# Kernel tuning notes

Hardware: AMD Instinct MI355X
Metric: run time of the kernel (lower is better)

## Reference

```python
import jax, jax.numpy as jnp
import numpy as np

C = 64          # channels
N = 500000      # points
FILTERS = (1, 3, 3, 3, 1)
INIT_SCALE = 8.0
LIKELIHOOD_BOUND = 1e-9


def setup_inputs() -> dict:
    key = jax.random.key(0)
    ks = jax.random.split(key, 6)
    inputs = jax.random.normal(ks[0], (N, C), jnp.float32) * 4.0
    # deterministic replacement for torch's np.random.uniform(-0.5, 0.5) noise
    noise = jax.random.uniform(ks[1], (N, C), jnp.float32, minval=-0.5, maxval=0.5)
    d = {"inputs": inputs, "noise": noise}
    scale = INIT_SCALE ** (1.0 / (len(FILTERS) - 1))  # init_scale**(1/4)
    for i in range(4):
        fo, fi = FILTERS[i + 1], FILTERS[i]
        init_m = float(np.log(np.expm1(1.0 / scale / fo)))
        d[f"m{i}"] = jnp.full((C, fo, fi), init_m, dtype=jnp.float32)
        d[f"b{i}"] = jax.random.uniform(ks[2 + i], (C, fo, 1), jnp.float32, minval=-0.5, maxval=0.5)
        d[f"f{i}"] = jnp.zeros((C, fo, 1), jnp.float32)
    return d


@jax.custom_vjp
def low_bound(x):
    return jnp.clip(x, LIKELIHOOD_BOUND)

def _lb_fwd(x):
    return jnp.clip(x, LIKELIHOOD_BOUND), x

def _lb_bwd(x, g):
    # torch Low_bound: grad zeroed where x < 1e-9 (the g<0 pass-through is
    # nullified by the preceding hard zeroing in the original code)
    return (jnp.where(x >= LIKELIHOOD_BOUND, g, jnp.zeros_like(g)),)

low_bound.defvjp(_lb_fwd, _lb_bwd)


def _logits_cumulative(x, ms, bs, fs):
    # x: (C, 1, N); each layer: tiny per-channel matmul + bias + tanh gate
    logits = x
    for m, b, f in zip(ms, bs, fs):
        logits = jnp.einsum('cij,cjn->cin', jax.nn.softplus(m), logits) + b
        logits = logits + jnp.tanh(f) * jnp.tanh(logits)
    return logits


def reference(inputs, noise, m0, m1, m2, m3, b0, b1, b2, b3, f0, f1, f2, f3):
    # quantize_mode='noise': additive uniform noise
    outputs = inputs + noise                       # (N, C)
    x = outputs.T[:, None, :]                      # (C, 1, N)
    ms = (m0, m1, m2, m3)
    bs = (b0, b1, b2, b3)
    fs = (f0, f1, f2, f3)
    lower = _logits_cumulative(x - 0.5, ms, bs, fs)   # (C, 1, N)
    upper = _logits_cumulative(x + 0.5, ms, bs, fs)   # (C, 1, N)
    sign = -jax.lax.stop_gradient(jnp.sign(lower + upper))
    likelihood = jnp.abs(jax.nn.sigmoid(sign * upper) - jax.nn.sigmoid(sign * lower))
    likelihood = likelihood.reshape(C, N).T        # (N, C)
    likelihood = low_bound(likelihood)
    return outputs, likelihood
```

## Files before the change

### kernel.cpp

```cpp
#include <hip/hip_runtime.h>

#define CH 64

__device__ __forceinline__ float frcp(float x) { return __builtin_amdgcn_rcpf(x); }

__device__ __forceinline__ float ftanh(float x) {
    float e = __expf(2.0f * x);
    return 1.0f - 2.0f * frcp(e + 1.0f);
}

__device__ __forceinline__ float softplus_f(float x) {
    float ax = fabsf(x);
    return fmaxf(x, 0.0f) + log1pf(__expf(-ax));
}

__device__ __forceinline__ float chain_gen(float x,
    const float* w0, const float* B0, const float* T0,
    const float* w1, const float* B1, const float* T1,
    const float* w2, const float* B2, const float* T2,
    const float* w3, float B3, float T3)
{
    float l[3], t[3];
#pragma unroll
    for (int i = 0; i < 3; i++) {
        float z = fmaf(w0[i], x, B0[i]);
        l[i] = fmaf(T0[i], ftanh(z), z);
    }
#pragma unroll
    for (int i = 0; i < 3; i++) {
        float z = B1[i];
#pragma unroll
        for (int j = 0; j < 3; j++) z = fmaf(w1[i * 3 + j], l[j], z);
        t[i] = fmaf(T1[i], ftanh(z), z);
    }
#pragma unroll
    for (int i = 0; i < 3; i++) {
        float z = B2[i];
#pragma unroll
        for (int j = 0; j < 3; j++) z = fmaf(w2[i * 3 + j], t[j], z);
        l[i] = fmaf(T2[i], ftanh(z), z);
    }
    float z = B3;
#pragma unroll
    for (int j = 0; j < 3; j++) z = fmaf(w3[j], l[j], z);
    return fmaf(T3, ftanh(z), z);
}

__device__ __forceinline__ float2 chain2_nogate(float xl, float xu,
    const float* w0, const float* B0,
    const float* w1, const float* B1,
    const float* w2, const float* B2,
    const float* w3, float B3)
{
    float lx[3], ly[3], tx[3], ty[3];
#pragma unroll
    for (int i = 0; i < 3; i++) {
        lx[i] = fmaf(w0[i], xl, B0[i]);
        ly[i] = fmaf(w0[i], xu, B0[i]);
    }
#pragma unroll
    for (int i = 0; i < 3; i++) {
        float zx = B1[i], zy = B1[i];
#pragma unroll
        for (int j = 0; j < 3; j++) {
            zx = fmaf(w1[i * 3 + j], lx[j], zx);
            zy = fmaf(w1[i * 3 + j], ly[j], zy);
        }
        tx[i] = zx; ty[i] = zy;
    }
#pragma unroll
    for (int i = 0; i < 3; i++) {
        float zx = B2[i], zy = B2[i];
#pragma unroll
        for (int j = 0; j < 3; j++) {
            zx = fmaf(w2[i * 3 + j], tx[j], zx);
            zy = fmaf(w2[i * 3 + j], ty[j], zy);
        }
        lx[i] = zx; ly[i] = zy;
    }
    float zx = B3, zy = B3;
#pragma unroll
    for (int j = 0; j < 3; j++) {
        zx = fmaf(w3[j], lx[j], zx);
        zy = fmaf(w3[j], ly[j], zy);
    }
    return make_float2(zx, zy);
}

__device__ __forceinline__ float likelihood_f(float lo, float up) {
    lo = fminf(fmaxf(lo, -40.0f), 40.0f);
    up = fminf(fmaxf(up, -40.0f), 40.0f);
    float a = __expf(-up);
    float b = __expf(-lo);
    float num = b - a;
    float den = fmaf(a, b, a) + b + 1.0f;
    float like = fabsf(num * frcp(den));
    return fmaxf(like, 1e-9f);
}

__global__ __launch_bounds__(256) void eb_kernel(
    const float* __restrict__ in, const float* __restrict__ noise,
    const float* __restrict__ m0, const float* __restrict__ b0, const float* __restrict__ f0,
    const float* __restrict__ m1, const float* __restrict__ b1, const float* __restrict__ f1,
    const float* __restrict__ m2, const float* __restrict__ b2, const float* __restrict__ f2,
    const float* __restrict__ m3, const float* __restrict__ b3, const float* __restrict__ f3,
    float* __restrict__ out, int total)
{
    const int tid = blockIdx.x * blockDim.x + threadIdx.x;
    const int c = tid & (CH - 1);

    float w0[3], B0[3], T0[3];
    float w1[9], B1[3], T1[3];
    float w2[9], B2[3], T2[3];
    float w3[3], B3, T3;
#pragma unroll
    for (int i = 0; i < 3; i++) {
        w0[i] = softplus_f(m0[c * 3 + i]);
        B0[i] = b0[c * 3 + i];
        T0[i] = tanhf(f0[c * 3 + i]);
        B1[i] = b1[c * 3 + i];
        T1[i] = tanhf(f1[c * 3 + i]);
        B2[i] = b2[c * 3 + i];
        T2[i] = tanhf(f2[c * 3 + i]);
        w3[i] = softplus_f(m3[c * 3 + i]);
    }
#pragma unroll
    for (int i = 0; i < 9; i++) {
        w1[i] = softplus_f(m1[c * 9 + i]);
        w2[i] = softplus_f(m2[c * 9 + i]);
    }
    B3 = b3[c];
    T3 = tanhf(f3[c]);

    bool gated = (T3 != 0.0f);
#pragma unroll
    for (int i = 0; i < 3; i++)
        gated = gated || (T0[i] != 0.0f) || (T1[i] != 0.0f) || (T2[i] != 0.0f);

    const int stride = gridDim.x * blockDim.x;

    if (!gated) {
        for (int idx = tid; idx < total; idx += stride) {
            float v = in[idx] + noise[idx];
            out[idx] = v;
            float2 r = chain2_nogate(v - 0.5f, v + 0.5f,
                                     w0, B0, w1, B1, w2, B2, w3, B3);
            out[total + idx] = likelihood_f(r.x, r.y);
        }
    } else {
        for (int idx = tid; idx < total; idx += stride) {
            float v = in[idx] + noise[idx];
            out[idx] = v;
            float lo = chain_gen(v - 0.5f, w0, B0, T0, w1, B1, T1, w2, B2, T2, w3, B3, T3);
            float up = chain_gen(v + 0.5f, w0, B0, T0, w1, B1, T1, w2, B2, T2, w3, B3, T3);
            out[total + idx] = likelihood_f(lo, up);
        }
    }
}

extern "C" void kernel_launch(void* const* d_in, const int* in_sizes, int n_in,
                              void* d_out, int out_size, void* d_ws, size_t ws_size,
                              hipStream_t stream) {
    const float* in    = (const float*)d_in[0];
    const float* noise = (const float*)d_in[1];
    const float* m0 = (const float*)d_in[2];
    const float* b0 = (const float*)d_in[3];
    const float* f0 = (const float*)d_in[4];
    const float* m1 = (const float*)d_in[5];
    const float* b1 = (const float*)d_in[6];
    const float* f1 = (const float*)d_in[7];
    const float* m2 = (const float*)d_in[8];
    const float* b2 = (const float*)d_in[9];
    const float* f2 = (const float*)d_in[10];
    const float* m3 = (const float*)d_in[11];
    const float* b3 = (const float*)d_in[12];
    const float* f3 = (const float*)d_in[13];
    float* out = (float*)d_out;

    const int total = in_sizes[0];
    const int threads = 256;
    const int blocks = 2048;

    eb_kernel<<<blocks, threads, 0, stream>>>(in, noise,
        m0, b0, f0, m1, b1, f1, m2, b2, f2, m3, b3, f3,
        out, total);
}
```

Measured before the change: 460.4 us.

## Collapse ungated affine chain to per-channel scalar and vectorize with float4

When every gate parameter is zero, the four-layer per-channel network reduces to an affine map. Each block now precomputes slope A and intercept D per channel into shared memory. The main loop evaluates the likelihood from a single exponential per element using float4 loads and stores, instead of running two full chains. It also computes the gate test block-wide from the raw f values, and tightens the clamp bound. The ungated path now assumes the total is a multiple of four and that the stride keeps channel alignment.

```diff
diff --git a/kernel.cpp b/kernel.cpp
--- a/kernel.cpp
+++ b/kernel.cpp
@@ -46,50 +46,9 @@
     return fmaf(T3, ftanh(z), z);
 }
 
-__device__ __forceinline__ float2 chain2_nogate(float xl, float xu,
-    const float* w0, const float* B0,
-    const float* w1, const float* B1,
-    const float* w2, const float* B2,
-    const float* w3, float B3)
-{
-    float lx[3], ly[3], tx[3], ty[3];
-#pragma unroll
-    for (int i = 0; i < 3; i++) {
-        lx[i] = fmaf(w0[i], xl, B0[i]);
-        ly[i] = fmaf(w0[i], xu, B0[i]);
-    }
-#pragma unroll
-    for (int i = 0; i < 3; i++) {
-        float zx = B1[i], zy = B1[i];
-#pragma unroll
-        for (int j = 0; j < 3; j++) {
-            zx = fmaf(w1[i * 3 + j], lx[j], zx);
-            zy = fmaf(w1[i * 3 + j], ly[j], zy);
-        }
-        tx[i] = zx; ty[i] = zy;
-    }
-#pragma unroll
-    for (int i = 0; i < 3; i++) {
-        float zx = B2[i], zy = B2[i];
-#pragma unroll
-        for (int j = 0; j < 3; j++) {
-            zx = fmaf(w2[i * 3 + j], tx[j], zx);
-            zy = fmaf(w2[i * 3 + j], ty[j], zy);
-        }
-        lx[i] = zx; ly[i] = zy;
-    }
-    float zx = B3, zy = B3;
-#pragma unroll
-    for (int j = 0; j < 3; j++) {
-        zx = fmaf(w3[j], lx[j], zx);
-        zy = fmaf(w3[j], ly[j], zy);
-    }
-    return make_float2(zx, zy);
-}
-
 __device__ __forceinline__ float likelihood_f(float lo, float up) {
-    lo = fminf(fmaxf(lo, -40.0f), 40.0f);
-    up = fminf(fmaxf(up, -40.0f), 40.0f);
+    lo = fminf(fmaxf(lo, -30.0f), 30.0f);
+    up = fminf(fmaxf(up, -30.0f), 30.0f);
     float a = __expf(-up);
     float b = __expf(-lo);
     float num = b - a;
@@ -106,48 +65,134 @@
     const float* __restrict__ m3, const float* __restrict__ b3, const float* __restrict__ f3,
     float* __restrict__ out, int total)
 {
-    const int tid = blockIdx.x * blockDim.x + threadIdx.x;
-    const int c = tid & (CH - 1);
-
-    float w0[3], B0[3], T0[3];
-    float w1[9], B1[3], T1[3];
-    float w2[9], B2[3], T2[3];
-    float w3[3], B3, T3;
-#pragma unroll
-    for (int i = 0; i < 3; i++) {
-        w0[i] = softplus_f(m0[c * 3 + i]);
-        B0[i] = b0[c * 3 + i];
-        T0[i] = tanhf(f0[c * 3 + i]);
-        B1[i] = b1[c * 3 + i];
-        T1[i] = tanhf(f1[c * 3 + i]);
-        B2[i] = b2[c * 3 + i];
-        T2[i] = tanhf(f2[c * 3 + i]);
-        w3[i] = softplus_f(m3[c * 3 + i]);
-    }
-#pragma unroll
-    for (int i = 0; i < 9; i++) {
-        w1[i] = softplus_f(m1[c * 9 + i]);
-        w2[i] = softplus_f(m2[c * 9 + i]);
-    }
-    B3 = b3[c];
-    T3 = tanhf(f3[c]);
-
-    bool gated = (T3 != 0.0f);
-#pragma unroll
-    for (int i = 0; i < 3; i++)
-        gated = gated || (T0[i] != 0.0f) || (T1[i] != 0.0f) || (T2[i] != 0.0f);
-
+    __shared__ float sA[CH];
+    __shared__ float sDm[CH];
+    __shared__ float sEA[CH];
+
+    const int t = threadIdx.x;
+    int localGate = 0;
+
+    if (t < CH) {
+        const int c = t;
+        float w0[3], B0[3], w1[9], B1[3], w2[9], B2[3], w3[3];
+#pragma unroll
+        for (int i = 0; i < 3; i++) {
+            w0[i] = softplus_f(m0[c * 3 + i]);
+            B0[i] = b0[c * 3 + i];
+            B1[i] = b1[c * 3 + i];
+            B2[i] = b2[c * 3 + i];
+            w3[i] = softplus_f(m3[c * 3 + i]);
+        }
+#pragma unroll
+        for (int i = 0; i < 9; i++) {
+            w1[i] = softplus_f(m1[c * 9 + i]);
+            w2[i] = softplus_f(m2[c * 9 + i]);
+        }
+        float B3 = b3[c];
+
+#pragma unroll
+        for (int i = 0; i < 3; i++)
+            localGate |= (f0[c * 3 + i] != 0.0f) | (f1[c * 3 + i] != 0.0f) | (f2[c * 3 + i] != 0.0f);
+        localGate |= (f3[c] != 0.0f);
+
+        float a0[3], d0[3], a1[3], d1[3], a2[3], d2[3];
+#pragma unroll
+        for (int i = 0; i < 3; i++) { a0[i] = w0[i]; d0[i] = B0[i]; }
+#pragma unroll
+        for (int i = 0; i < 3; i++) {
+            float za = 0.0f, zd = B1[i];
+#pragma unroll
+            for (int j = 0; j < 3; j++) {
+                za = fmaf(w1[i * 3 + j], a0[j], za);
+                zd = fmaf(w1[i * 3 + j], d0[j], zd);
+            }
+            a1[i] = za; d1[i] = zd;
+        }
+#pragma unroll
+        for (int i = 0; i < 3; i++) {
+            float za = 0.0f, zd = B2[i];
+#pragma unroll
+            for (int j = 0; j < 3; j++) {
+                za = fmaf(w2[i * 3 + j], a1[j], za);
+                zd = fmaf(w2[i * 3 + j], d1[j], zd);
+            }
+            a2[i] = za; d2[i] = zd;
+        }
+        float A = 0.0f, D = B3;
+#pragma unroll
+        for (int j = 0; j < 3; j++) {
+            A = fmaf(w3[j], a2[j], A);
+            D = fmaf(w3[j], d2[j], D);
+        }
+        sA[c]  = A;
+        sDm[c] = D - 0.5f * A;
+        sEA[c] = __expf(-A);
+    }
+
+    const int anyGate = __syncthreads_or(localGate);
+
+    const int tid = blockIdx.x * blockDim.x + t;
     const int stride = gridDim.x * blockDim.x;
 
-    if (!gated) {
-        for (int idx = tid; idx < total; idx += stride) {
-            float v = in[idx] + noise[idx];
-            out[idx] = v;
-            float2 r = chain2_nogate(v - 0.5f, v + 0.5f,
-                                     w0, B0, w1, B1, w2, B2, w3, B3);
-            out[total + idx] = likelihood_f(r.x, r.y);
+    if (!anyGate) {
+        const int n4 = total >> 2;
+        const int c0 = (tid << 2) & (CH - 1);
+        float A[4], Dm[4], EA[4], K1[4], K2[4];
+#pragma unroll
+        for (int k = 0; k < 4; k++) {
+            A[k]  = sA[c0 + k];
+            Dm[k] = sDm[c0 + k];
+            EA[k] = sEA[c0 + k];
+            K1[k] = 1.0f - EA[k];
+            K2[k] = 1.0f + EA[k];
+        }
+        const float4* in4    = (const float4*)in;
+        const float4* noise4 = (const float4*)noise;
+        float4* out4  = (float4*)out;
+        float4* like4 = (float4*)(out + total);
+
+        for (int idx = tid; idx < n4; idx += stride) {
+            float4 a = in4[idx];
+            float4 nz = noise4[idx];
+            float v[4] = { a.x + nz.x, a.y + nz.y, a.z + nz.z, a.w + nz.w };
+            out4[idx] = make_float4(v[0], v[1], v[2], v[3]);
+            float lk[4];
+#pragma unroll
+            for (int k = 0; k < 4; k++) {
+                float lo = fmaf(A[k], v[k], Dm[k]);
+                lo = fminf(fmaxf(lo, -30.0f), 30.0f);
+                float b  = __expf(-lo);
+                float den = fmaf(b * EA[k], b, fmaf(b, K2[k], 1.0f));
+                float lkv = (b * K1[k]) * frcp(den);
+                lk[k] = fmaxf(lkv, 1e-9f);
+            }
+            like4[idx] = make_float4(lk[0], lk[1], lk[2], lk[3]);
         }
     } else {
+        const int c = tid & (CH - 1);
+        float w0[3], B0[3], T0[3];
+        float w1[9], B1[3], T1[3];
+        float w2[9], B2[3], T2[3];
+        float w3[3], B3, T3;
+#pragma unroll
+        for (int i = 0; i < 3; i++) {
+            w0[i] = softplus_f(m0[c * 3 + i]);
+            B0[i] = b0[c * 3 + i];
+            T0[i] = tanhf(f0[c * 3 + i]);
+            B1[i] = b1[c * 3 + i];
+            T1[i] = tanhf(f1[c * 3 + i]);
+            B2[i] = b2[c * 3 + i];
+            T2[i] = tanhf(f2[c * 3 + i]);
+            w3[i] = softplus_f(m3[c * 3 + i]);
+        }
+#pragma unroll
+        for (int i = 0; i < 9; i++) {
+            w1[i] = softplus_f(m1[c * 9 + i]);
+            w2[i] = softplus_f(m2[c * 9 + i]);
+        }
+        B3 = b3[c];
+        T3 = tanhf(f3[c]);
+
         for (int idx = tid; idx < total; idx += stride) {
             float v = in[idx] + noise[idx];
             out[idx] = v;
```

Result: no change. 453.0 us (-1.6%).
